# Kernel optimization log

Hardware: AMD Instinct MI355X
Metric: run time of the kernel (lower is better)

Reference implementation:

```python
import jax, jax.numpy as jnp
import numpy as np

EMBED = 1024
HEADS = 16
HEAD_DIM = EMBED // HEADS
BATCH = 4
SEQ = 2048


def setup_inputs() -> dict:
    key = jax.random.key(0)
    ks = jax.random.split(key, 9)
    s = 1.0 / np.sqrt(EMBED)
    inp = {
        "x": jax.random.normal(ks[0], (BATCH, SEQ, EMBED), dtype=jnp.float32),
        "Wq": jax.random.normal(ks[1], (EMBED, EMBED), dtype=jnp.float32) * s,
        "bq": jnp.zeros((EMBED,), jnp.float32),
        "Wk": jax.random.normal(ks[2], (EMBED, EMBED), dtype=jnp.float32) * s,
        "bk": jnp.zeros((EMBED,), jnp.float32),
        "Wv": jax.random.normal(ks[3], (EMBED, EMBED), dtype=jnp.float32) * s,
        "bv": jnp.zeros((EMBED,), jnp.float32),
        "Wo": jax.random.normal(ks[4], (EMBED, EMBED), dtype=jnp.float32) * s,
        "bo": jnp.zeros((EMBED,), jnp.float32),
    }
    return inp


def reference(x, Wq, bq, Wk, bk, Wv, bv, Wo, bo):
    B, S, E = x.shape
    H, D = HEADS, HEAD_DIM
    # projections (torch Linear with weight stored as [in,out] here)
    q = (x @ Wq + bq).reshape(B, S, H, D).transpose(0, 2, 1, 3)  # [B,H,S,D]
    k = (x @ Wk + bk).reshape(B, S, H, D).transpose(0, 2, 1, 3)
    v = (x @ Wv + bv).reshape(B, S, H, D).transpose(0, 2, 1, 3)
    scores = jnp.einsum('bhqd,bhkd->bhqk', q, k) * (1.0 / np.sqrt(D))
    causal = jnp.tril(jnp.ones((S, S), dtype=bool))
    scores = jnp.where(causal[None, None], scores, -jnp.inf)
    attn = jax.nn.softmax(scores, axis=-1)  # dropout p=0.0 -> identity
    out = jnp.einsum('bhqk,bhkd->bhqd', attn, v)  # [B,H,S,D]
    out = out.transpose(0, 2, 1, 3).reshape(B, S, E)
    return out @ Wo + bo
```

## Files before the change

### kernel.cpp

```cpp
#include <hip/hip_runtime.h>
#include <stdint.h>

#define EMBED 1024
#define SEQ   2048
#define BATCH 4
#define HEADS 16
#define HDIM  64
#define LDP   72

typedef unsigned short ushort_t;
typedef __bf16 bf16x8 __attribute__((ext_vector_type(8)));
typedef ushort_t u16x8 __attribute__((ext_vector_type(8)));
typedef float  f32x4  __attribute__((ext_vector_type(4)));

#define MFMA16 __builtin_amdgcn_mfma_f32_16x16x32_bf16

typedef __attribute__((address_space(3))) uint32_t lds_u32_t;
typedef __attribute__((address_space(1))) const uint32_t glb_u32_t;

__device__ __forceinline__ void gl_lds16(const ushort_t* g, ushort_t* l) {
    __builtin_amdgcn_global_load_lds((glb_u32_t*)g, (lds_u32_t*)l, 16, 0, 0);
}

__device__ __forceinline__ ushort_t f2bf(float f) {
    union { float f; uint32_t u; } c; c.f = f;
    uint32_t u = c.u;
    return (ushort_t)((u + 0x7FFFu + ((u >> 16) & 1u)) >> 16);
}

__global__ __launch_bounds__(256)
void cast_x(const float* __restrict__ X, ushort_t* __restrict__ Xb)
{
    size_t i = ((size_t)blockIdx.x * 256 + threadIdx.x) * 8;
    ushort_t tmp[8];
    #pragma unroll
    for (int e = 0; e < 8; ++e) tmp[e] = f2bf(X[i + e]);
    *(uint4*)(Xb + i) = *(const uint4*)tmp;
}

__global__ __launch_bounds__(256)
void cast_transpose_w(const float* __restrict__ W, ushort_t* __restrict__ Wt)
{
    __shared__ ushort_t Ts[64 * 80];
    const int t = threadIdx.x;
    const int k0 = blockIdx.x * 64, n0 = blockIdx.y * 64;
    const int r = t >> 2, cs = (t & 3) * 16;
    const float* src = W + (size_t)(k0 + r) * EMBED + n0 + cs;
    #pragma unroll
    for (int e = 0; e < 16; ++e) Ts[(cs + e) * 80 + r] = f2bf(src[e]);
    __syncthreads();
    const int n = t >> 2, ks = (t & 3) * 16;
    ushort_t* dst = Wt + (size_t)(n0 + n) * EMBED + k0 + ks;
    *(uint4*)(dst)     = *(const uint4*)(&Ts[n * 80 + ks]);
    *(uint4*)(dst + 8) = *(const uint4*)(&Ts[n * 80 + ks + 8]);
}

__global__ __launch_bounds__(256)
void gemm_qkv(const ushort_t* __restrict__ A, const ushort_t* __restrict__ Bt,
              const float* __restrict__ bq, const float* __restrict__ bk,
              const float* __restrict__ bv, ushort_t* __restrict__ Cq, size_t tsz)
{
    __shared__ ushort_t As[128 * 32];
    __shared__ ushort_t Bs[128 * 32];
    const int t = threadIdx.x;
    const int wave = t >> 6, lane = t & 63;
    const int l15 = lane & 15, quad = lane >> 4;
    const int m0 = blockIdx.y * 128, n0 = blockIdx.x * 128;
    const int wm = (wave >> 1) * 64, wn = (wave & 1) * 64;
    f32x4 acc[4][4] = {};

    const int srow = wave * 32 + (lane >> 2), scol = (lane & 3) * 8;
    const ushort_t* Ag = A  + (size_t)(m0 + srow) * EMBED + scol;
    const ushort_t* Bg = Bt + (size_t)(n0 + srow) * EMBED + scol;
    ushort_t* AsW = As + wave * 1024;
    ushort_t* BsW = Bs + wave * 1024;

    for (int k0 = 0; k0 < EMBED; k0 += 32) {
        gl_lds16(Ag + k0,              AsW);
        gl_lds16(Ag + k0 + 16 * EMBED, AsW + 512);
        gl_lds16(Bg + k0,              BsW);
        gl_lds16(Bg + k0 + 16 * EMBED, BsW + 512);
        __syncthreads();

        bf16x8 af[4], bfr[4];
        #pragma unroll
        for (int mt = 0; mt < 4; ++mt)
            af[mt] = *(const bf16x8*)(&As[(wm + mt * 16 + l15) * 32 + quad * 8]);
        #pragma unroll
        for (int nt = 0; nt < 4; ++nt)
            bfr[nt] = *(const bf16x8*)(&Bs[(wn + nt * 16 + l15) * 32 + quad * 8]);
        #pragma unroll
        for (int mt = 0; mt < 4; ++mt)
            #pragma unroll
            for (int nt = 0; nt < 4; ++nt)
                acc[mt][nt] = MFMA16(af[mt], bfr[nt], acc[mt][nt], 0, 0, 0);
        __syncthreads();
    }

    const int mat = blockIdx.x >> 3;
    const float* bias = (mat == 0) ? bq : (mat == 1) ? bk : bv;
    const float scale = (mat == 0) ? 0.125f : 1.0f;
    ushort_t* C = Cq + (size_t)mat * tsz;
    const int nc0 = (blockIdx.x & 7) * 128;
    #pragma unroll
    for (int nt = 0; nt < 4; ++nt) {
        int col = nc0 + wn + nt * 16 + l15;
        float bb = bias[col];
        #pragma unroll
        for (int mt = 0; mt < 4; ++mt)
            #pragma unroll
            for (int r = 0; r < 4; ++r) {
                int row = m0 + wm + mt * 16 + quad * 4 + r;
                C[(size_t)row * EMBED + col] = f2bf((acc[mt][nt][r] + bb) * scale);
            }
    }
}

__global__ __launch_bounds__(256)
void gemm_o(const ushort_t* __restrict__ A, const ushort_t* __restrict__ Bt,
            const float* __restrict__ bias, float* __restrict__ C)
{
    __shared__ ushort_t As[128 * 32];
    __shared__ ushort_t Bs[128 * 32];
    const int t = threadIdx.x;
    const int wave = t >> 6, lane = t & 63;
    const int l15 = lane & 15, quad = lane >> 4;
    const int m0 = blockIdx.y * 128, n0 = blockIdx.x * 128;
    const int wm = (wave >> 1) * 64, wn = (wave & 1) * 64;
    f32x4 acc[4][4] = {};

    const int srow = wave * 32 + (lane >> 2), scol = (lane & 3) * 8;
    const ushort_t* Ag = A  + (size_t)(m0 + srow) * EMBED + scol;
    const ushort_t* Bg = Bt + (size_t)(n0 + srow) * EMBED + scol;
    ushort_t* AsW = As + wave * 1024;
    ushort_t* BsW = Bs + wave * 1024;

    for (int k0 = 0; k0 < EMBED; k0 += 32) {
        gl_lds16(Ag + k0,              AsW);
        gl_lds16(Ag + k0 + 16 * EMBED, AsW + 512);
        gl_lds16(Bg + k0,              BsW);
        gl_lds16(Bg + k0 + 16 * EMBED, BsW + 512);
        __syncthreads();

        bf16x8 af[4], bfr[4];
        #pragma unroll
        for (int mt = 0; mt < 4; ++mt)
            af[mt] = *(const bf16x8*)(&As[(wm + mt * 16 + l15) * 32 + quad * 8]);
        #pragma unroll
        for (int nt = 0; nt < 4; ++nt)
            bfr[nt] = *(const bf16x8*)(&Bs[(wn + nt * 16 + l15) * 32 + quad * 8]);
        #pragma unroll
        for (int mt = 0; mt < 4; ++mt)
            #pragma unroll
            for (int nt = 0; nt < 4; ++nt)
                acc[mt][nt] = MFMA16(af[mt], bfr[nt], acc[mt][nt], 0, 0, 0);
        __syncthreads();
    }

    #pragma unroll
    for (int nt = 0; nt < 4; ++nt) {
        int col = n0 + wn + nt * 16 + l15;
        float bb = bias[col];
        #pragma unroll
        for (int mt = 0; mt < 4; ++mt)
            #pragma unroll
            for (int r = 0; r < 4; ++r) {
                int row = m0 + wm + mt * 16 + quad * 4 + r;
                C[(size_t)row * EMBED + col] = acc[mt][nt][r] + bb;
            }
    }
}

__global__ __launch_bounds__(256)
void transpose_v(const ushort_t* __restrict__ V, ushort_t* __restrict__ Vt)
{
    int blk = blockIdx.x;
    int st = blk & 31, bh = blk >> 5;
    int h = bh & 15, b = bh >> 4;
    int s0 = st * 64;
    __shared__ ushort_t Ts[64 * LDP];
    int tid = threadIdx.x;
    int r = tid >> 2, g = (tid & 3) * 8;

    const ushort_t* src = V + ((size_t)(b * SEQ + s0 + r)) * EMBED + h * HDIM;
    uint4 v0 = *(const uint4*)(src + g);
    uint4 v1 = *(const uint4*)(src + g + 32);
    const ushort_t* e0 = (const ushort_t*)&v0;
    const ushort_t* e1 = (const ushort_t*)&v1;
    #pragma unroll
    for (int e = 0; e < 8; ++e) Ts[(g + e) * LDP + r] = e0[e];
    #pragma unroll
    for (int e = 0; e < 8; ++e) Ts[(g + 32 + e) * LDP + r] = e1[e];
    __syncthreads();

    int d = tid >> 2;
    ushort_t* dst = Vt + ((size_t)bh * HDIM + d) * SEQ + s0;
    *(uint4*)(dst + g)      = *(const uint4*)(&Ts[d * LDP + g]);
    *(uint4*)(dst + g + 32) = *(const uint4*)(&Ts[d * LDP + g + 32]);
}

__global__ __launch_bounds__(256)
void flash_attn(const ushort_t* __restrict__ Q, const ushort_t* __restrict__ K,
                const ushort_t* __restrict__ Vt, ushort_t* __restrict__ O)
{
    const int blk = blockIdx.x;
    const int p = blk & 15, bh = blk >> 4;
    const int h = bh & 15, b = bh >> 4;
    const int t = threadIdx.x, wave = t >> 6, lane = t & 63;
    const int l15 = lane & 15, quad = lane >> 4;
    const int i0m[2] = { p * 64 + wave * 16, (31 - p) * 64 + wave * 16 };
    const int lastj[2] = { p, 31 - p };
    const size_t qkbase = (size_t)b * SEQ * EMBED + (size_t)h * HDIM;
    const size_t vtbase = (size_t)bh * HDIM * SEQ;

    __shared__ ushort_t Ks[64 * LDP];
    __shared__ ushort_t Vs[64 * LDP];
    __shared__ ushort_t Ps[4][32 * LDP];
    ushort_t* psw = &Ps[wave][0];

    bf16x8 qa[2][2];
    #pragma unroll
    for (int mt = 0; mt < 2; ++mt)
        #pragma unroll
        for (int ks = 0; ks < 2; ++ks)
            qa[mt][ks] = *(const bf16x8*)(Q + qkbase + (size_t)(i0m[mt] + l15) * EMBED + ks * 32 + quad * 8);

    union { uint32_t u[4]; bf16x8 v; } onesu;
    onesu.u[0] = onesu.u[1] = onesu.u[2] = onesu.u[3] = 0x3F803F80u;
    const bf16x8 ones = onesu.v;

    const int tr = t >> 2, tseg = (t & 3) * 16;
    const ushort_t* Kg = K  + qkbase + (size_t)tr * EMBED + tseg;
    const ushort_t* Vg = Vt + vtbase + (size_t)tr * SEQ + tseg;
    ushort_t* KsT = &Ks[tr * LDP + tseg];
    ushort_t* VsT = &Vs[tr * LDP + tseg];

    const int lastjb = 31 - p;
    uint4 ka0 = *(const uint4*)(Kg);
    uint4 ka1 = *(const uint4*)(Kg + 8);
    uint4 va0 = *(const uint4*)(Vg);
    uint4 va1 = *(const uint4*)(Vg + 8);

    f32x4 o_acc[2][4] = {};
    f32x4 l_acc[2] = {};

    for (int jt = 0; jt <= lastjb; ++jt) {
        *(uint4*)(KsT)     = ka0;
        *(uint4*)(KsT + 8) = ka1;
        *(uint4*)(VsT)     = va0;
        *(uint4*)(VsT + 8) = va1;
        if (jt < lastjb) {
            const ushort_t* Kn = Kg + (size_t)(jt + 1) * 64 * EMBED;
            const ushort_t* Vn = Vg + (size_t)(jt + 1) * 64;
            ka0 = *(const uint4*)(Kn);
            ka1 = *(const uint4*)(Kn + 8);
            va0 = *(const uint4*)(Vn);
            va1 = *(const uint4*)(Vn + 8);
        }
        __syncthreads();

        const int j0 = jt * 64;
        const bool act0 = (jt <= lastj[0]);

        f32x4 s[2][4] = {};
        #pragma unroll
        for (int ks = 0; ks < 2; ++ks)
            #pragma unroll
            for (int ct = 0; ct < 4; ++ct) {
                bf16x8 kb = *(const bf16x8*)(&Ks[(ct * 16 + l15) * LDP + ks * 32 + quad * 8]);
                if (act0) s[0][ct] = MFMA16(qa[0][ks], kb, s[0][ct], 0, 0, 0);
                s[1][ct] = MFMA16(qa[1][ks], kb, s[1][ct], 0, 0, 0);
            }

        #pragma unroll
        for (int mt = 0; mt < 2; ++mt) {
            if (mt == 0 && !act0) continue;
            if (jt == lastj[mt]) {
                #pragma unroll
                for (int ct = 0; ct < 4; ++ct)
                    #pragma unroll
                    for (int r = 0; r < 4; ++r) {
                        float pv = __expf(s[mt][ct][r]);
                        if (j0 + ct * 16 + l15 > i0m[mt] + quad * 4 + r) pv = 0.f;
                        union { float f; uint32_t u; } cv; cv.f = pv;
                        psw[(mt * 16 + quad * 4 + r) * LDP + ct * 16 + l15] = (ushort_t)(cv.u >> 16);
                    }
            } else {
                #pragma unroll
                for (int ct = 0; ct < 4; ++ct)
                    #pragma unroll
                    for (int r = 0; r < 4; ++r) {
                        float pv = __expf(s[mt][ct][r]);
                        union { float f; uint32_t u; } cv; cv.f = pv;
                        psw[(mt * 16 + quad * 4 + r) * LDP + ct * 16 + l15] = (ushort_t)(cv.u >> 16);
                    }
            }
        }

        #pragma unroll
        for (int mt = 0; mt < 2; ++mt) {
            if (mt == 0 && !act0) continue;
            #pragma unroll
            for (int ks = 0; ks < 2; ++ks) {
                union { u16x8 s; bf16x8 b; } pr;
                pr.s = *(const u16x8*)(&psw[(mt * 16 + l15) * LDP + ks * 32 + quad * 8]);
                bf16x8 pa = pr.b;
                l_acc[mt] = MFMA16(pa, ones, l_acc[mt], 0, 0, 0);
                #pragma unroll
                for (int dt = 0; dt < 4; ++dt) {
                    bf16x8 vb = *(const bf16x8*)(&Vs[(dt * 16 + l15) * LDP + ks * 32 + quad * 8]);
                    o_acc[mt][dt] = MFMA16(pa, vb, o_acc[mt][dt], 0, 0, 0);
                }
            }
        }
        __syncthreads();
    }

    #pragma unroll
    for (int mt = 0; mt < 2; ++mt)
        #pragma unroll
        for (int r = 0; r < 4; ++r) {
            float invl = 1.f / l_acc[mt][r];
            size_t ob = qkbase + (size_t)(i0m[mt] + quad * 4 + r) * EMBED;
            #pragma unroll
            for (int dt = 0; dt < 4; ++dt)
                O[ob + dt * 16 + l15] = f2bf(o_acc[mt][dt][r] * invl);
        }
}

extern "C" void kernel_launch(void* const* d_in, const int* in_sizes, int n_in,
                              void* d_out, int out_size, void* d_ws, size_t ws_size,
                              hipStream_t stream)
{
    (void)in_sizes; (void)n_in; (void)out_size; (void)ws_size;
    const float* x  = (const float*)d_in[0];
    const float* Wq = (const float*)d_in[1];
    const float* bq = (const float*)d_in[2];
    const float* Wk = (const float*)d_in[3];
    const float* bk = (const float*)d_in[4];
    const float* Wv = (const float*)d_in[5];
    const float* bv = (const float*)d_in[6];
    const float* Wo = (const float*)d_in[7];
    const float* bo = (const float*)d_in[8];
    float* out = (float*)d_out;

    const int M = BATCH * SEQ;
    size_t tsz = (size_t)M * EMBED;
    size_t wsz = (size_t)EMBED * EMBED;
    ushort_t* xb  = (ushort_t*)d_ws;
    ushort_t* Qb  = xb + tsz;
    ushort_t* Kb  = Qb + tsz;
    ushort_t* Vb  = Kb + tsz;
    ushort_t* Vt  = Vb + tsz;
    ushort_t* Wt0 = Vt + tsz;
    ushort_t* Wt1 = Wt0 + wsz;
    ushort_t* Wt2 = Wt1 + wsz;
    ushort_t* Wt3 = Wt2 + wsz;
    ushort_t* Ob  = xb;

    dim3 wg(16, 16);
    cast_x<<<4096, 256, 0, stream>>>(x, xb);
    cast_transpose_w<<<wg, 256, 0, stream>>>(Wq, Wt0);
    cast_transpose_w<<<wg, 256, 0, stream>>>(Wk, Wt1);
    cast_transpose_w<<<wg, 256, 0, stream>>>(Wv, Wt2);
    cast_transpose_w<<<wg, 256, 0, stream>>>(Wo, Wt3);

    gemm_qkv<<<dim3(24, 64), 256, 0, stream>>>(xb, Wt0, bq, bk, bv, Qb, tsz);

    transpose_v<<<BATCH * HEADS * (SEQ / 64), 256, 0, stream>>>(Vb, Vt);
    flash_attn<<<BATCH * HEADS * (SEQ / 128), 256, 0, stream>>>(Qb, Kb, Vt, Ob);

    gemm_o<<<dim3(8, 64), 256, 0, stream>>>(Ob, Wt3, bo, out);
}
```

Baseline: 299.7 us.

## Restructure flash attention with 32x32 MFMA, async LDS double-buffering, exp2 scores

Rewrites the attention kernel so each wave owns 32 query rows and computes S^T with 32x32x16 MFMAs, keeping P in registers as the A operand for the PV product instead of staging it through LDS. K/V tiles are loaded straight to swizzled LDS with global_load_lds into a double buffer, and the row sum is accumulated in registers rather than by an extra MFMA against ones. The Q scale folds in log2(e) so the native v_exp_f32 (exp2) can be used, and blocks are remapped so the heaviest causal tiles are scheduled first. It drops the max subtraction (as before) and relies on the swizzle and LDS read of Ls being correct without a barrier.

```diff
diff --git a/kernel.cpp b/kernel.cpp
--- a/kernel.cpp
+++ b/kernel.cpp
@@ -10,10 +10,12 @@
 
 typedef unsigned short ushort_t;
 typedef __bf16 bf16x8 __attribute__((ext_vector_type(8)));
-typedef ushort_t u16x8 __attribute__((ext_vector_type(8)));
+typedef __bf16 bf16x4 __attribute__((ext_vector_type(4)));
 typedef float  f32x4  __attribute__((ext_vector_type(4)));
+typedef float  f32x16 __attribute__((ext_vector_type(16)));
 
 #define MFMA16 __builtin_amdgcn_mfma_f32_16x16x32_bf16
+#define MFMA32 __builtin_amdgcn_mfma_f32_32x32x16_bf16
 
 typedef __attribute__((address_space(3))) uint32_t lds_u32_t;
 typedef __attribute__((address_space(1))) const uint32_t glb_u32_t;
@@ -26,6 +28,10 @@
     union { float f; uint32_t u; } c; c.f = f;
     uint32_t u = c.u;
     return (ushort_t)((u + 0x7FFFu + ((u >> 16) & 1u)) >> 16);
+}
+
+__device__ __forceinline__ float exp2f_fast(float x) {
+    float r; asm("v_exp_f32 %0, %1" : "=v"(r) : "v"(x)); return r;
 }
 
 __global__ __launch_bounds__(256)
@@ -99,7 +105,7 @@
 
     const int mat = blockIdx.x >> 3;
     const float* bias = (mat == 0) ? bq : (mat == 1) ? bk : bv;
-    const float scale = (mat == 0) ? 0.125f : 1.0f;
+    const float scale = (mat == 0) ? 0.18033688011112042f : 1.0f;
     ushort_t* C = Cq + (size_t)mat * tsz;
     const int nc0 = (blockIdx.x & 7) * 128;
     #pragma unroll
@@ -203,129 +209,139 @@
 void flash_attn(const ushort_t* __restrict__ Q, const ushort_t* __restrict__ K,
                 const ushort_t* __restrict__ Vt, ushort_t* __restrict__ O)
 {
-    const int blk = blockIdx.x;
-    const int p = blk & 15, bh = blk >> 4;
+    const int logical = (blockIdx.x & 7) * 128 + (blockIdx.x >> 3);
+    const int bh = logical >> 4;
+    const int pb = 15 - (logical & 15);
     const int h = bh & 15, b = bh >> 4;
-    const int t = threadIdx.x, wave = t >> 6, lane = t & 63;
-    const int l15 = lane & 15, quad = lane >> 4;
-    const int i0m[2] = { p * 64 + wave * 16, (31 - p) * 64 + wave * 16 };
-    const int lastj[2] = { p, 31 - p };
+    const int t = threadIdx.x, w = t >> 6, lane = t & 63;
+    const int l31 = lane & 31, hi = lane >> 5;
+    const int s = pb * 4 + w;
+    const int sdiag = s >> 1;
+    const int lastJt = 2 * pb + 1;
     const size_t qkbase = (size_t)b * SEQ * EMBED + (size_t)h * HDIM;
     const size_t vtbase = (size_t)bh * HDIM * SEQ;
 
-    __shared__ ushort_t Ks[64 * LDP];
-    __shared__ ushort_t Vs[64 * LDP];
-    __shared__ ushort_t Ps[4][32 * LDP];
-    ushort_t* psw = &Ps[wave][0];
-
-    bf16x8 qa[2][2];
-    #pragma unroll
-    for (int mt = 0; mt < 2; ++mt)
-        #pragma unroll
-        for (int ks = 0; ks < 2; ++ks)
-            qa[mt][ks] = *(const bf16x8*)(Q + qkbase + (size_t)(i0m[mt] + l15) * EMBED + ks * 32 + quad * 8);
-
-    union { uint32_t u[4]; bf16x8 v; } onesu;
-    onesu.u[0] = onesu.u[1] = onesu.u[2] = onesu.u[3] = 0x3F803F80u;
-    const bf16x8 ones = onesu.v;
-
-    const int tr = t >> 2, tseg = (t & 3) * 16;
-    const ushort_t* Kg = K  + qkbase + (size_t)tr * EMBED + tseg;
-    const ushort_t* Vg = Vt + vtbase + (size_t)tr * SEQ + tseg;
-    ushort_t* KsT = &Ks[tr * LDP + tseg];
-    ushort_t* VsT = &Vs[tr * LDP + tseg];
-
-    const int lastjb = 31 - p;
-    uint4 ka0 = *(const uint4*)(Kg);
-    uint4 ka1 = *(const uint4*)(Kg + 8);
-    uint4 va0 = *(const uint4*)(Vg);
-    uint4 va1 = *(const uint4*)(Vg + 8);
-
-    f32x4 o_acc[2][4] = {};
-    f32x4 l_acc[2] = {};
-
-    for (int jt = 0; jt <= lastjb; ++jt) {
-        *(uint4*)(KsT)     = ka0;
-        *(uint4*)(KsT + 8) = ka1;
-        *(uint4*)(VsT)     = va0;
-        *(uint4*)(VsT + 8) = va1;
-        if (jt < lastjb) {
-            const ushort_t* Kn = Kg + (size_t)(jt + 1) * 64 * EMBED;
-            const ushort_t* Vn = Vg + (size_t)(jt + 1) * 64;
-            ka0 = *(const uint4*)(Kn);
-            ka1 = *(const uint4*)(Kn + 8);
-            va0 = *(const uint4*)(Vn);
-            va1 = *(const uint4*)(Vn + 8);
+    __shared__ ushort_t KsB[2][64 * 64];
+    __shared__ ushort_t VsB[2][64 * 64];
+    __shared__ float Ls[4][32];
+
+    bf16x8 qb[4];
+    const ushort_t* qrow = Q + qkbase + (size_t)(s * 32 + l31) * EMBED + hi * 8;
+    #pragma unroll
+    for (int ks = 0; ks < 4; ++ks)
+        qb[ks] = *(const bf16x8*)(qrow + ks * 16);
+
+    const int rr = lane >> 3, cc = lane & 7;
+    const ushort_t* KgL = K  + qkbase + (size_t)(w * 16 + rr) * EMBED + ((cc ^ rr) * 8);
+    const ushort_t* VgL = Vt + vtbase + (size_t)(w * 16 + rr) * SEQ  + ((cc ^ rr) * 8);
+
+    f32x16 o0 = {}, o1 = {};
+    float l_part = 0.f;
+
+    {
+        ushort_t* kd = &KsB[0][w * 1024];
+        ushort_t* vd = &VsB[0][w * 1024];
+        gl_lds16(KgL,             kd);
+        gl_lds16(KgL + 8 * EMBED, kd + 512);
+        gl_lds16(VgL,             vd);
+        gl_lds16(VgL + 8 * SEQ,   vd + 512);
+    }
+
+    int cur = 0;
+    for (int jt = 0; jt <= lastJt; ++jt) {
+        __syncthreads();
+
+        if (jt < lastJt) {
+            const ushort_t* kg = KgL + (size_t)(jt + 1) * 64 * EMBED;
+            const ushort_t* vg = VgL + (jt + 1) * 64;
+            ushort_t* kd = &KsB[cur ^ 1][w * 1024];
+            ushort_t* vd = &VsB[cur ^ 1][w * 1024];
+            gl_lds16(kg,             kd);
+            gl_lds16(kg + 8 * EMBED, kd + 512);
+            gl_lds16(vg,             vd);
+            gl_lds16(vg + 8 * SEQ,   vd + 512);
         }
-        __syncthreads();
-
-        const int j0 = jt * 64;
-        const bool act0 = (jt <= lastj[0]);
-
-        f32x4 s[2][4] = {};
-        #pragma unroll
-        for (int ks = 0; ks < 2; ++ks)
-            #pragma unroll
-            for (int ct = 0; ct < 4; ++ct) {
-                bf16x8 kb = *(const bf16x8*)(&Ks[(ct * 16 + l15) * LDP + ks * 32 + quad * 8]);
-                if (act0) s[0][ct] = MFMA16(qa[0][ks], kb, s[0][ct], 0, 0, 0);
-                s[1][ct] = MFMA16(qa[1][ks], kb, s[1][ct], 0, 0, 0);
-            }
-
-        #pragma unroll
-        for (int mt = 0; mt < 2; ++mt) {
-            if (mt == 0 && !act0) continue;
-            if (jt == lastj[mt]) {
-                #pragma unroll
-                for (int ct = 0; ct < 4; ++ct)
-                    #pragma unroll
-                    for (int r = 0; r < 4; ++r) {
-                        float pv = __expf(s[mt][ct][r]);
-                        if (j0 + ct * 16 + l15 > i0m[mt] + quad * 4 + r) pv = 0.f;
-                        union { float f; uint32_t u; } cv; cv.f = pv;
-                        psw[(mt * 16 + quad * 4 + r) * LDP + ct * 16 + l15] = (ushort_t)(cv.u >> 16);
-                    }
-            } else {
-                #pragma unroll
-                for (int ct = 0; ct < 4; ++ct)
-                    #pragma unroll
-                    for (int r = 0; r < 4; ++r) {
-                        float pv = __expf(s[mt][ct][r]);
-                        union { float f; uint32_t u; } cv; cv.f = pv;
-                        psw[(mt * 16 + quad * 4 + r) * LDP + ct * 16 + l15] = (ushort_t)(cv.u >> 16);
-                    }
+
+        if (jt <= sdiag) {
+            const ushort_t* Kst = &KsB[cur][0];
+            const ushort_t* Vst = &VsB[cur][0];
+            const bool dg = (jt == sdiag);
+            const bool skip1 = dg && !(s & 1);
+            const bool mask0 = dg && !(s & 1);
+            const bool mask1 = dg && (s & 1);
+            const int swz = l31 & 7;
+
+            f32x16 st0 = {}, st1 = {};
+            #pragma unroll
+            for (int ks = 0; ks < 4; ++ks) {
+                bf16x8 ka = *(const bf16x8*)(Kst + l31 * 64 + (((ks * 2 + hi) ^ swz) * 8));
+                st0 = MFMA32(ka, qb[ks], st0, 0, 0, 0);
+            }
+            if (!skip1) {
+                #pragma unroll
+                for (int ks = 0; ks < 4; ++ks) {
+                    bf16x8 ka = *(const bf16x8*)(Kst + (32 + l31) * 64 + (((ks * 2 + hi) ^ swz) * 8));
+                    st1 = MFMA32(ka, qb[ks], st1, 0, 0, 0);
+                }
+            }
+
+            bf16x8 pa0 = {}, pa1 = {}, pa2 = {}, pa3 = {};
+            {
+                float p[16];
+                #pragma unroll
+                for (int r = 0; r < 16; ++r) {
+                    float pv = exp2f_fast(st0[r]);
+                    int key = (r & 3) + 8 * (r >> 2) + 4 * hi;
+                    pv = (mask0 && key > l31) ? 0.f : pv;
+                    p[r] = pv; l_part += pv;
+                }
+                #pragma unroll
+                for (int e = 0; e < 8; ++e) { pa0[e] = (__bf16)p[e]; pa1[e] = (__bf16)p[8 + e]; }
+            }
+            if (!skip1) {
+                float p[16];
+                #pragma unroll
+                for (int r = 0; r < 16; ++r) {
+                    float pv = exp2f_fast(st1[r]);
+                    int key = (r & 3) + 8 * (r >> 2) + 4 * hi;
+                    pv = (mask1 && key > l31) ? 0.f : pv;
+                    p[r] = pv; l_part += pv;
+                }
+                #pragma unroll
+                for (int e = 0; e < 8; ++e) { pa2[e] = (__bf16)p[e]; pa3[e] = (__bf16)p[8 + e]; }
+            }
+
+            #pragma unroll
+            for (int ksl = 0; ksl < 4; ++ksl) {
+                if (!(ksl >= 2 && skip1)) {
+                    bf16x8 pf = (ksl == 0) ? pa0 : (ksl == 1) ? pa1 : (ksl == 2) ? pa2 : pa3;
+                    const int c0 = (((ksl * 2)     ^ swz) * 8) + hi * 4;
+                    const int c1 = (((ksl * 2 + 1) ^ swz) * 8) + hi * 4;
+                    union { bf16x4 hh[2]; bf16x8 v; } u0, u1;
+                    u0.hh[0] = *(const bf16x4*)(Vst + l31 * 64 + c0);
+                    u0.hh[1] = *(const bf16x4*)(Vst + l31 * 64 + c1);
+                    u1.hh[0] = *(const bf16x4*)(Vst + (32 + l31) * 64 + c0);
+                    u1.hh[1] = *(const bf16x4*)(Vst + (32 + l31) * 64 + c1);
+                    o0 = MFMA32(pf, u0.v, o0, 0, 0, 0);
+                    o1 = MFMA32(pf, u1.v, o1, 0, 0, 0);
+                }
             }
         }
-
-        #pragma unroll
-        for (int mt = 0; mt < 2; ++mt) {
-            if (mt == 0 && !act0) continue;
-            #pragma unroll
-            for (int ks = 0; ks < 2; ++ks) {
-                union { u16x8 s; bf16x8 b; } pr;
-                pr.s = *(const u16x8*)(&psw[(mt * 16 + l15) * LDP + ks * 32 + quad * 8]);
-                bf16x8 pa = pr.b;
-                l_acc[mt] = MFMA16(pa, ones, l_acc[mt], 0, 0, 0);
-                #pragma unroll
-                for (int dt = 0; dt < 4; ++dt) {
-                    bf16x8 vb = *(const bf16x8*)(&Vs[(dt * 16 + l15) * LDP + ks * 32 + quad * 8]);
-                    o_acc[mt][dt] = MFMA16(pa, vb, o_acc[mt][dt], 0, 0, 0);
-                }
-            }
-        }
-        __syncthreads();
-    }
-
-    #pragma unroll
-    for (int mt = 0; mt < 2; ++mt)
-        #pragma unroll
-        for (int r = 0; r < 4; ++r) {
-            float invl = 1.f / l_acc[mt][r];
-            size_t ob = qkbase + (size_t)(i0m[mt] + quad * 4 + r) * EMBED;
-            #pragma unroll
-            for (int dt = 0; dt < 4; ++dt)
-                O[ob + dt * 16 + l15] = f2bf(o_acc[mt][dt][r] * invl);
-        }
+        cur ^= 1;
+    }
+
+    float ltot = l_part + __shfl_xor(l_part, 32);
+
+    if (!hi) Ls[w][l31] = ltot;
+
+    #pragma unroll
+    for (int r = 0; r < 16; ++r) {
+        int q = (r & 3) + 8 * (r >> 2) + 4 * hi;
+        float linv = 1.0f / Ls[w][q];
+        size_t ob = qkbase + (size_t)(s * 32 + q) * EMBED;
+        O[ob + l31]      = f2bf(o0[r] * linv);
+        O[ob + 32 + l31] = f2bf(o1[r] * linv);
+    }
 }
 
 extern "C" void kernel_launch(void* const* d_in, const int* in_sizes, int n_in,
```

After: 285.6 us. -4.7%, faster.
